# Kernel tuning notes

Hardware: AMD Instinct MI355X
Metric: run time of the kernel (lower is better)

Reference implementation:

```python
import jax, jax.numpy as jnp
import numpy as np

N = 50000
E = 500000
NODE_F = 128
POS_F = 3
COORD_F = 64
EDGE_IN = 2 * NODE_F + 1  # 257


def _linear_params(key, fan_in, fan_out):
    k1, k2 = jax.random.split(key)
    bound = 1.0 / np.sqrt(fan_in)
    W = jax.random.uniform(k1, (fan_in, fan_out), jnp.float32, -bound, bound)
    b = jax.random.uniform(k2, (fan_out,), jnp.float32, -bound, bound)
    return W, b


def setup_inputs() -> dict:
    key = jax.random.key(0)
    ks = jax.random.split(key, 8)
    x = jax.random.normal(ks[0], (N, NODE_F + POS_F), jnp.float32)
    edge_index = jax.random.randint(ks[1], (2, E), 0, N, jnp.int64)
    W_e1, b_e1 = _linear_params(ks[2], EDGE_IN, 2 * EDGE_IN)
    W_e2, b_e2 = _linear_params(ks[3], 2 * EDGE_IN, COORD_F)
    W_c1, b_c1 = _linear_params(ks[4], COORD_F, 4 * COORD_F)
    W_c2, b_c2 = _linear_params(ks[5], 4 * COORD_F, 1)
    W_n1, b_n1 = _linear_params(ks[6], NODE_F + COORD_F, 2 * NODE_F)
    W_n2, b_n2 = _linear_params(ks[7], 2 * NODE_F, NODE_F)
    return {"x": x, "edge_index": edge_index,
            "W_e1": W_e1, "b_e1": b_e1, "W_e2": W_e2, "b_e2": b_e2,
            "W_c1": W_c1, "b_c1": b_c1, "W_c2": W_c2, "b_c2": b_c2,
            "W_n1": W_n1, "b_n1": b_n1, "W_n2": W_n2, "b_n2": b_n2}


def reference(x, edge_index, W_e1, b_e1, W_e2, b_e2, W_c1, b_c1, W_c2, b_c2,
              W_n1, b_n1, W_n2, b_n2):
    node = x[:, :-POS_F]            # (N, 128)
    coords = x[:, -POS_F:]          # (N, 3)
    src = edge_index[0]             # j (source)
    dst = edge_index[1]             # i (target)

    rel_coords = coords[src] - coords[dst]                          # (E, 3)
    rel_dist = jnp.sqrt(jnp.sum(rel_coords ** 2, -1, keepdims=True))  # (E, 1)

    # message: edge_mlp(cat[x_i, x_j, edge_attr])
    e_in = jnp.concatenate([node[dst], node[src], rel_dist], axis=-1)  # (E, 257)
    h = jax.nn.silu(e_in @ W_e1 + b_e1)
    m_ij = jax.nn.silu(h @ W_e2 + b_e2)                             # (E, 64)
    coord_w = jax.nn.silu(m_ij @ W_c1 + b_c1) @ W_c2 + b_c2         # (E, 1)

    # scatter-sum aggregation to target nodes
    m_i = jax.ops.segment_sum(m_ij, dst, num_segments=N)            # (N, 64)
    w_i = jax.ops.segment_sum(coord_w, dst, num_segments=N)         # (N, 1)
    r_i = jax.ops.segment_sum(rel_coords, dst, num_segments=N)      # (N, 3)

    coords_out = coords + w_i * r_i
    n_in = jnp.concatenate([node, m_i], axis=-1)                    # (N, 192)
    hidden = jax.nn.silu(n_in @ W_n1 + b_n1) @ W_n2 + b_n2 + node   # (N, 128)
    return jnp.concatenate([hidden, coords_out], axis=-1)           # (N, 131)
```

## Files before the change

kernel.cpp:

```cpp
#include <hip/hip_runtime.h>
#include <hip/hip_bf16.h>
#include <hip/hip_fp16.h>

#define NN 50000
#define NE 500000
#define DCAP 48

using bf16x8 = __attribute__((ext_vector_type(8))) short;
using f16x8  = __attribute__((ext_vector_type(8))) _Float16;
using f32x4  = __attribute__((ext_vector_type(4))) float;

__device__ __forceinline__ float b2f(unsigned short s) {
  union { unsigned u; float f; } v; v.u = ((unsigned)s) << 16; return v.f;
}
__device__ __forceinline__ unsigned short f2b(float f) {
  __hip_bfloat16 h = __float2bfloat16(f);
  return *reinterpret_cast<unsigned short*>(&h);
}
__device__ __forceinline__ unsigned short f2h(float f) {
  __half h = __float2half(f);
  return *reinterpret_cast<unsigned short*>(&h);
}
__device__ __forceinline__ float hu2f(unsigned short s) {
  __half h; *reinterpret_cast<unsigned short*>(&h) = s; return __half2float(h);
}
__device__ __forceinline__ unsigned pack2(float a, float b) {
  __hip_bfloat162 h = __float22bfloat162_rn(make_float2(a, b));
  return *reinterpret_cast<unsigned*>(&h);
}
__device__ __forceinline__ unsigned pack2h(float a, float b) {
  __half2 h = __float22half2_rn(make_float2(a, b));
  return *reinterpret_cast<unsigned*>(&h);
}
__device__ __forceinline__ __half2 h2u(unsigned u) {
  union { unsigned v; __half2 h; } x; x.v = u; return x.h;
}
__device__ __forceinline__ float silu_f(float x) {
  return x * __fdividef(1.f, 1.f + __expf(-x));
}

__global__ void prep_weights(const float* __restrict__ we1,
                             const float* __restrict__ be1,
                             const float* __restrict__ we2,
                             const float* __restrict__ be2,
                             const float* __restrict__ wc1,
                             const float* __restrict__ wn1,
                             const float* __restrict__ wn2,
                             unsigned short* __restrict__ A1p,
                             unsigned short* __restrict__ A2p,
                             unsigned short* __restrict__ AdB,
                             unsigned short* __restrict__ W2p,
                             unsigned short* __restrict__ Wc1p,
                             unsigned short* __restrict__ Wn1p,
                             unsigned short* __restrict__ Wn2p,
                             float* __restrict__ be1p) {
  int i = blockIdx.x * 256 + threadIdx.x;
  if (i < 67584) {
    int n = i / 128, k = i % 128;
    A1p[i] = (n < 514) ? f2b(we1[k * 514 + n]) : (unsigned short)0;
  } else if (i < 135168) {
    int j = i - 67584; int n = j / 128, k = j % 128;
    A2p[j] = (n < 514) ? f2b(we1[(128 + k) * 514 + n]) : (unsigned short)0;
  } else if (i < 135696) {
    int j = i - 135168;
    AdB[j] = (j < 514) ? f2h(we1[256 * 514 + j]) : (unsigned short)0;
  } else if (i < 170512) {
    int j = i - 135696; int n = j / 544, lk = j % 544;
    unsigned short v = 0;
    if (lk < 514) v = f2h(we2[lk * 64 + n]);
    else if (lk == 514) v = f2h(be2[n]);
    W2p[j] = v;
  } else if (i < 186896) {
    int j = i - 170512; int n = j / 64, k = j % 64;
    Wc1p[j] = f2b(wc1[k * 256 + n]);
  } else if (i < 236048) {
    int j = i - 186896; int n = j / 192, k = j % 192;
    Wn1p[j] = f2b(wn1[k * 256 + n]);
  } else if (i < 268816) {
    int j = i - 236048; int n = j / 256, k = j % 256;
    Wn2p[j] = f2b(wn2[k * 128 + n]);
  } else if (i < 269344) {
    int j = i - 268816;
    be1p[j] = (j < 514) ? be1[j] : 0.f;
  }
}

__global__ void prep_nodes(const float* __restrict__ x,
                           unsigned short* __restrict__ node_p,
                           float* __restrict__ coords_p) {
  int i = blockIdx.x * 256 + threadIdx.x;
  if (i < NN * 16) {
    int g = i >> 4, c = i & 15;
    const float* s = x + g * 131 + c * 8;
    unsigned short* d = node_p + g * 128 + c * 8;
#pragma unroll
    for (int j = 0; j < 8; j++) d[j] = f2b(s[j]);
  } else if (i < NN * 16 + NN) {
    int g = i - NN * 16;
    float4 c;
    c.x = x[g * 131 + 128];
    c.y = x[g * 131 + 129];
    c.z = x[g * 131 + 130];
    c.w = 0.f;
    *(float4*)(coords_p + g * 4) = c;
  }
}

__global__ void build_adj(const int* __restrict__ eidx,
                          int* __restrict__ cnt, int* __restrict__ adj) {
  int e = blockIdx.x * 256 + threadIdx.x;
  if (e < NE) {
    int d = eidx[NE + e];
    d = min(max(d, 0), NN - 1);
    int slot = atomicAdd(&cnt[d], 1);
    if (slot < DCAP) adj[d * DCAP + slot] = e;
  }
}

__launch_bounds__(256, 2)
__global__ void pgemm_kernel(const unsigned short* __restrict__ node_p,
                             const unsigned short* __restrict__ A1p,
                             const unsigned short* __restrict__ A2p,
                             const float* __restrict__ be1p,
                             unsigned short* __restrict__ P1,
                             unsigned short* __restrict__ P2) {
  __shared__ unsigned short sNode[64][136];
  int tid = threadIdx.x, blk = blockIdx.x;
  int lane = tid & 63, wv = tid >> 6, l16 = lane & 15, quad = lane >> 4;
#pragma unroll
  for (int it = 0; it < 4; it++) {
    int t = tid + it * 256;
    int row = t >> 4, ch = t & 15;
    int g = blk * 64 + row;
    if (g >= NN) g = 0;
    *(bf16x8*)(&sNode[row][ch * 8]) = *(const bf16x8*)(node_p + g * 128 + ch * 8);
  }
  __syncthreads();
#pragma unroll 1
  for (int t = 0; t < 9; t++) {
    int T = wv + 4 * t;
    if (T >= 33) break;
    f32x4 a1[4], a2[4];
#pragma unroll
    for (int s = 0; s < 4; s++) {
      a1[s] = (f32x4){0.f, 0.f, 0.f, 0.f};
      a2[s] = (f32x4){0.f, 0.f, 0.f, 0.f};
    }
    for (int kb = 0; kb < 4; kb++) {
      bf16x8 b1 = *(const bf16x8*)(A1p + (T * 16 + l16) * 128 + kb * 32 + quad * 8);
      bf16x8 b2 = *(const bf16x8*)(A2p + (T * 16 + l16) * 128 + kb * 32 + quad * 8);
#pragma unroll
      for (int s = 0; s < 4; s++) {
        bf16x8 a = *(const bf16x8*)(&sNode[s * 16 + l16][kb * 32 + quad * 8]);
        a1[s] = __builtin_amdgcn_mfma_f32_16x16x32_bf16(b1, a, a1[s], 0, 0, 0);
        a2[s] = __builtin_amdgcn_mfma_f32_16x16x32_bf16(b2, a, a2[s], 0, 0, 0);
      }
    }
    int nb = T * 16 + quad * 4;
    float4 b4 = *(const float4*)(be1p + nb);
    bool v0 = nb + 0 < 514, v1 = nb + 1 < 514, v2 = nb + 2 < 514, v3 = nb + 3 < 514;
#pragma unroll
    for (int s = 0; s < 4; s++) {
      int g = blk * 64 + s * 16 + l16;
      if (g < NN) {
        float p0 = v0 ? a1[s][0] + b4.x : 0.f;
        float p1v = v1 ? a1[s][1] + b4.y : 0.f;
        float p2v = v2 ? a1[s][2] + b4.z : 0.f;
        float p3 = v3 ? a1[s][3] + b4.w : 0.f;
        *(uint2*)(P1 + g * 528 + nb) = make_uint2(pack2h(p0, p1v), pack2h(p2v, p3));
        float q0 = v0 ? a2[s][0] : 0.f;
        float q1 = v1 ? a2[s][1] : 0.f;
        float q2 = v2 ? a2[s][2] : 0.f;
        float q3 = v3 ? a2[s][3] : 0.f;
        *(uint2*)(P2 + g * 528 + nb) = make_uint2(pack2h(q0, q1), pack2h(q2, q3));
      }
    }
  }
}

__launch_bounds__(256, 3)
__global__ void edge_kernel(const unsigned short* __restrict__ P1,
                            const unsigned short* __restrict__ P2,
                            const unsigned short* __restrict__ AdB,
                            const float* __restrict__ coords_p,
                            const int* __restrict__ eidx,
                            const unsigned short* __restrict__ W2p,
                            const unsigned short* __restrict__ Wc1p,
                            const float* __restrict__ bc1,
                            const float* __restrict__ bc2,
                            const float* __restrict__ wc2,
                            unsigned short* __restrict__ medge,
                            float* __restrict__ coordw) {
  __shared__ unsigned short sHc[48][168];
  __shared__ unsigned short sM[48][72];
  __shared__ int sDst[48];
  __shared__ int sSrc[48];
  __shared__ float sDistF[48];
  __shared__ float sCwPart[4][48];
  int tid = threadIdx.x, blk = blockIdx.x;
  int lane = tid & 63, wv = tid >> 6, l16 = lane & 15, quad = lane >> 4;

  if (tid < 48) {
    int e = min(blk * 48 + tid, NE - 1);
    int s = eidx[e], d = eidx[NE + e];
    s = min(max(s, 0), NN - 1);
    d = min(max(d, 0), NN - 1);
    float4 cs = *(const float4*)(coords_p + s * 4);
    float4 cd = *(const float4*)(coords_p + d * 4);
    float rx = cs.x - cd.x, ry = cs.y - cd.y, rz = cs.z - cd.z;
    sDst[tid] = d;
    sSrc[tid] = s;
    sDistF[tid] = sqrtf(rx * rx + ry * ry + rz * rz);
  }
  __syncthreads();

  int cg = tid & 15, er = tid >> 4;
  const unsigned short* p1b[3];
  const unsigned short* p2b[3];
  __half2 d2[3];
#pragma unroll
  for (int it = 0; it < 3; it++) {
    int edge = er + it * 16;
    p1b[it] = P1 + sDst[edge] * 528 + cg * 8;
    p2b[it] = P2 + sSrc[edge] * 528 + cg * 8;
    d2[it] = __float2half2_rn(sDistF[edge]);
  }
  const unsigned short* adB = AdB + cg * 8;
  const unsigned short* w2b = W2p + (wv * 16 + l16) * 544 + quad * 8;

  f32x4 macc[3];
#pragma unroll
  for (int s = 0; s < 3; s++) macc[s] = (f32x4){0.f, 0.f, 0.f, 0.f};

#pragma unroll
  for (int ch = 0; ch < 4; ch++) {
    uint4 uva = *(const uint4*)(adB + ch * 128);
    __half2 va0 = h2u(uva.x), va1 = h2u(uva.y), va2 = h2u(uva.z), va3 = h2u(uva.w);
#pragma unroll
    for (int it = 0; it < 3; it++) {
      int edge = er + it * 16;
      uint4 u1 = *(const uint4*)(p1b[it] + ch * 128);
      uint4 u2 = *(const uint4*)(p2b[it] + ch * 128);
      __half2 z0 = __hfma2(va0, d2[it], __hadd2(h2u(u1.x), h2u(u2.x)));
      __half2 z1 = __hfma2(va1, d2[it], __hadd2(h2u(u1.y), h2u(u2.y)));
      __half2 z2 = __hfma2(va2, d2[it], __hadd2(h2u(u1.z), h2u(u2.z)));
      __half2 z3 = __hfma2(va3, d2[it], __hadd2(h2u(u1.w), h2u(u2.w)));
      float f0 = __low2float(z0), f1 = __high2float(z0);
      float f2 = __low2float(z1), f3 = __high2float(z1);
      float f4 = __low2float(z2), f5 = __high2float(z2);
      float f6 = __low2float(z3), f7 = __high2float(z3);
      *(uint4*)(&sHc[edge][cg * 8]) = make_uint4(
          pack2h(silu_f(f0), silu_f(f1)), pack2h(silu_f(f2), silu_f(f3)),
          pack2h(silu_f(f4), silu_f(f5)), pack2h(silu_f(f6), silu_f(f7)));
    }
    if (ch == 3 && tid < 48) {
      int edge = tid;
      float dist = sDistF[edge];
      int bd = sDst[edge] * 528, bs = sSrc[edge] * 528;
      float h512 = silu_f(hu2f(P1[bd + 512]) + hu2f(P2[bs + 512]) + dist * hu2f(AdB[512]));
      float h513 = silu_f(hu2f(P1[bd + 513]) + hu2f(P2[bs + 513]) + dist * hu2f(AdB[513]));
      *(uint4*)(&sHc[edge][128]) = make_uint4(pack2h(h512, h513), pack2h(1.0f, 0.f), 0u, 0u);
      *(uint4*)(&sHc[edge][136]) = make_uint4(0u, 0u, 0u, 0u);
      *(uint4*)(&sHc[edge][144]) = make_uint4(0u, 0u, 0u, 0u);
      *(uint4*)(&sHc[edge][152]) = make_uint4(0u, 0u, 0u, 0u);
    }
    __syncthreads();
    const int nkb = (ch == 3) ? 5 : 4;
#pragma unroll
    for (int kb = 0; kb < nkb; kb++) {
      f16x8 b = *(const f16x8*)(w2b + ch * 128 + kb * 32);
#pragma unroll
      for (int s = 0; s < 3; s++) {
        f16x8 a = *(const f16x8*)(&sHc[s * 16 + l16][kb * 32 + quad * 8]);
        macc[s] = __builtin_amdgcn_mfma_f32_16x16x32_f16(b, a, macc[s], 0, 0, 0);
      }
    }
    __syncthreads();
  }

  {
    int nb = wv * 16 + quad * 4;
#pragma unroll
    for (int s = 0; s < 3; s++) {
      unsigned lo = pack2(silu_f(macc[s][0]), silu_f(macc[s][1]));
      unsigned hi = pack2(silu_f(macc[s][2]), silu_f(macc[s][3]));
      *(uint2*)(&sM[s * 16 + l16][nb]) = make_uint2(lo, hi);
    }
  }
  __syncthreads();

  {
    float cw[3] = {0.f, 0.f, 0.f};
#pragma unroll
    for (int jt = 0; jt < 4; jt++) {
      int T = wv * 4 + jt;
      f32x4 cacc[3];
#pragma unroll
      for (int s = 0; s < 3; s++) cacc[s] = (f32x4){0.f, 0.f, 0.f, 0.f};
#pragma unroll
      for (int kb = 0; kb < 2; kb++) {
        bf16x8 b = *(const bf16x8*)(Wc1p + (T * 16 + l16) * 64 + kb * 32 + quad * 8);
#pragma unroll
        for (int s = 0; s < 3; s++) {
          bf16x8 a = *(const bf16x8*)(&sM[s * 16 + l16][kb * 32 + quad * 8]);
          cacc[s] = __builtin_amdgcn_mfma_f32_16x16x32_bf16(b, a, cacc[s], 0, 0, 0);
        }
      }
      int nb = T * 16 + quad * 4;
      float4 b4 = *(const float4*)(bc1 + nb);
      float4 w4 = *(const float4*)(wc2 + nb);
#pragma unroll
      for (int s = 0; s < 3; s++) {
        cw[s] += silu_f(cacc[s][0] + b4.x) * w4.x;
        cw[s] += silu_f(cacc[s][1] + b4.y) * w4.y;
        cw[s] += silu_f(cacc[s][2] + b4.z) * w4.z;
        cw[s] += silu_f(cacc[s][3] + b4.w) * w4.w;
      }
    }
#pragma unroll
    for (int s = 0; s < 3; s++) {
      cw[s] += __shfl_xor(cw[s], 16, 64);
      cw[s] += __shfl_xor(cw[s], 32, 64);
    }
    if (quad == 0) {
#pragma unroll
      for (int s = 0; s < 3; s++) sCwPart[wv][s * 16 + l16] = cw[s];
    }
  }
  __syncthreads();
#pragma unroll
  for (int it = 0; it < 2; it++) {
    int idx = it * 256 + tid;
    if (idx < 384) {
      int row = idx >> 3, ch8 = idx & 7;
      int e = blk * 48 + row;
      if (e < NE)
        *(bf16x8*)(medge + (size_t)e * 64 + ch8 * 8) = *(const bf16x8*)(&sM[row][ch8 * 8]);
    }
  }
  if (tid < 48) {
    int e = blk * 48 + tid;
    if (e < NE) {
      float v = sCwPart[0][tid] + sCwPart[1][tid] + sCwPart[2][tid] + sCwPart[3][tid]
                + bc2[0];
      coordw[e] = v;
    }
  }
}

__global__ void gather_kernel(const float* __restrict__ coords_p,
                              const unsigned short* __restrict__ medge,
                              const float* __restrict__ coordw,
                              const int* __restrict__ eidx,
                              const int* __restrict__ cnt,
                              const int* __restrict__ adj,
                              float* __restrict__ m_i,
                              float* __restrict__ wr) {
  int t = blockIdx.x * 256 + threadIdx.x;
  int g = t >> 2, c = t & 3;
  if (g >= NN) return;
  int deg = min(cnt[g], DCAP);
  float acc[16];
#pragma unroll
  for (int i = 0; i < 16; i++) acc[i] = 0.f;
  float sc = 0.f;
  float cg = (c < 3) ? coords_p[g * 4 + c] : 0.f;
  for (int k = 0; k < deg; k++) {
    int e = adj[g * DCAP + k];
    const unsigned short* mrow = medge + (size_t)e * 64 + c * 16;
    bf16x8 a0 = *(const bf16x8*)(mrow);
    bf16x8 a1 = *(const bf16x8*)(mrow + 8);
#pragma unroll
    for (int i = 0; i < 8; i++) acc[i] += b2f((unsigned short)a0[i]);
#pragma unroll
    for (int i = 0; i < 8; i++) acc[8 + i] += b2f((unsigned short)a1[i]);
    if (c == 3) {
      sc += coordw[e];
    } else {
      int s = eidx[e];
      s = min(max(s, 0), NN - 1);
      sc += coords_p[s * 4 + c] - cg;
    }
  }
  float4* dst = (float4*)(m_i + g * 64 + c * 16);
  dst[0] = make_float4(acc[0], acc[1], acc[2], acc[3]);
  dst[1] = make_float4(acc[4], acc[5], acc[6], acc[7]);
  dst[2] = make_float4(acc[8], acc[9], acc[10], acc[11]);
  dst[3] = make_float4(acc[12], acc[13], acc[14], acc[15]);
  wr[g * 4 + c] = sc;
}

__launch_bounds__(256, 2)
__global__ void node_mlp_kernel(const unsigned short* __restrict__ node_p,
                                const float* __restrict__ x,
                                const float* __restrict__ coords_p,
                                const float* __restrict__ m_i,
                                const float* __restrict__ wr,
                                const unsigned short* __restrict__ Wn1p,
                                const unsigned short* __restrict__ Wn2p,
                                const float* __restrict__ bn1,
                                const float* __restrict__ bn2,
                                float* __restrict__ out) {
  __shared__ unsigned short sNin[64][200];
  __shared__ unsigned short sHid[64][264];
  int tid = threadIdx.x, blk = blockIdx.x;
  int lane = tid & 63, wv = tid >> 6, l16 = lane & 15, quad = lane >> 4;

#pragma unroll
  for (int it = 0; it < 4; it++) {
    int t = tid + it * 256;
    int row = t >> 4, ch = t & 15;
    int g = blk * 64 + row;
    if (g >= NN) g = 0;
    *(bf16x8*)(&sNin[row][ch * 8]) = *(const bf16x8*)(node_p + g * 128 + ch * 8);
  }
#pragma unroll
  for (int it = 0; it < 2; it++) {
    int t = tid + it * 256;
    int row = t >> 3, q = t & 7;
    int g = blk * 64 + row;
    if (g >= NN) g = 0;
    float4 v1 = *(const float4*)(m_i + g * 64 + q * 8);
    float4 v2 = *(const float4*)(m_i + g * 64 + q * 8 + 4);
    *(uint2*)(&sNin[row][128 + q * 8]) = make_uint2(pack2(v1.x, v1.y), pack2(v1.z, v1.w));
    *(uint2*)(&sNin[row][128 + q * 8 + 4]) = make_uint2(pack2(v2.x, v2.y), pack2(v2.z, v2.w));
  }
  __syncthreads();
  {
    f32x4 acc[4][4];
#pragma unroll
    for (int j = 0; j < 4; j++)
#pragma unroll
      for (int s = 0; s < 4; s++) acc[j][s] = (f32x4){0.f, 0.f, 0.f, 0.f};
    for (int kb = 0; kb < 6; kb++) {
      bf16x8 afr[4], bfr[4];
#pragma unroll
      for (int s = 0; s < 4; s++)
        afr[s] = *(const bf16x8*)(&sNin[s * 16 + l16][kb * 32 + quad * 8]);
#pragma unroll
      for (int j = 0; j < 4; j++)
        bfr[j] = *(const bf16x8*)(Wn1p + ((wv * 4 + j) * 16 + l16) * 192 + kb * 32 + quad * 8);
#pragma unroll
      for (int j = 0; j < 4; j++)
#pragma unroll
        for (int s = 0; s < 4; s++)
          acc[j][s] = __builtin_amdgcn_mfma_f32_16x16x32_bf16(bfr[j], afr[s], acc[j][s], 0, 0, 0);
    }
#pragma unroll
    for (int j = 0; j < 4; j++) {
      int nb = (wv * 4 + j) * 16 + quad * 4;
      float4 b4 = *(const float4*)(bn1 + nb);
#pragma unroll
      for (int s = 0; s < 4; s++) {
        unsigned lo = pack2(silu_f(acc[j][s][0] + b4.x), silu_f(acc[j][s][1] + b4.y));
        unsigned hi = pack2(silu_f(acc[j][s][2] + b4.z), silu_f(acc[j][s][3] + b4.w));
        *(uint2*)(&sHid[s * 16 + l16][nb]) = make_uint2(lo, hi);
      }
    }
  }
  __syncthreads();
  {
    f32x4 acc[2][4];
#pragma unroll
    for (int j = 0; j < 2; j++)
#pragma unroll
      for (int s = 0; s < 4; s++) acc[j][s] = (f32x4){0.f, 0.f, 0.f, 0.f};
    for (int kb = 0; kb < 8; kb++) {
      bf16x8 afr[4], bfr[2];
#pragma unroll
      for (int s = 0; s < 4; s++)
        afr[s] = *(const bf16x8*)(&sHid[s * 16 + l16][kb * 32 + quad * 8]);
#pragma unroll
      for (int j = 0; j < 2; j++)
        bfr[j] = *(const bf16x8*)(Wn2p + ((wv * 2 + j) * 16 + l16) * 256 + kb * 32 + quad * 8);
#pragma unroll
      for (int j = 0; j < 2; j++)
#pragma unroll
        for (int s = 0; s < 4; s++)
          acc[j][s] = __builtin_amdgcn_mfma_f32_16x16x32_bf16(bfr[j], afr[s], acc[j][s], 0, 0, 0);
    }
#pragma unroll
    for (int j = 0; j < 2; j++) {
      int nb = (wv * 2 + j) * 16 + quad * 4;
      float4 b4 = *(const float4*)(bn2 + nb);
#pragma unroll
      for (int s = 0; s < 4; s++) {
        int g = blk * 64 + s * 16 + l16;
        if (g < NN) {
          int base = g * 131 + nb;
          out[base + 0] = acc[j][s][0] + b4.x + x[base + 0];
          out[base + 1] = acc[j][s][1] + b4.y + x[base + 1];
          out[base + 2] = acc[j][s][2] + b4.z + x[base + 2];
          out[base + 3] = acc[j][s][3] + b4.w + x[base + 3];
        }
      }
    }
  }
  if (tid < 64) {
    int g = blk * 64 + tid;
    if (g < NN) {
      float4 w4 = *(const float4*)(wr + g * 4);
      out[g * 131 + 128] = coords_p[g * 4 + 0] + w4.w * w4.x;
      out[g * 131 + 129] = coords_p[g * 4 + 1] + w4.w * w4.y;
      out[g * 131 + 130] = coords_p[g * 4 + 2] + w4.w * w4.z;
    }
  }
}

extern "C" void kernel_launch(void* const* d_in, const int* in_sizes, int n_in,
                              void* d_out, int out_size, void* d_ws, size_t ws_size,
                              hipStream_t stream) {
  const float* x   = (const float*)d_in[0];
  const int* eidx  = (const int*)d_in[1];
  const float* we1 = (const float*)d_in[2];
  const float* be1 = (const float*)d_in[3];
  const float* we2 = (const float*)d_in[4];
  const float* be2 = (const float*)d_in[5];
  const float* wc1 = (const float*)d_in[6];
  const float* bc1 = (const float*)d_in[7];
  const float* wc2 = (const float*)d_in[8];
  const float* bc2 = (const float*)d_in[9];
  const float* wn1 = (const float*)d_in[10];
  const float* bn1 = (const float*)d_in[11];
  const float* wn2 = (const float*)d_in[12];
  const float* bn2 = (const float*)d_in[13];

  char* ws = (char*)d_ws;
  unsigned short* A1p    = (unsigned short*)(ws + 0);
  unsigned short* A2p    = (unsigned short*)(ws + 135168);
  unsigned short* AdB    = (unsigned short*)(ws + 270336);
  unsigned short* W2p    = (unsigned short*)(ws + 271392);
  unsigned short* Wc1p   = (unsigned short*)(ws + 341024);
  unsigned short* Wn1p   = (unsigned short*)(ws + 373792);
  unsigned short* Wn2p   = (unsigned short*)(ws + 472096);
  float* be1p            = (float*)(ws + 537632);
  unsigned short* node_p = (unsigned short*)(ws + 539744);
  float* coords_p        = (float*)(ws + 13339744);
  unsigned short* medge  = (unsigned short*)(ws + 14139744);
  float* coordw          = (float*)(ws + 78139744);
  int* cnt               = (int*)(ws + 80139744);
  int* adj               = (int*)(ws + 80339744);
  float* m_i             = (float*)(ws + 89939744);
  float* wr              = (float*)(ws + 102739744);
  unsigned short* P1     = (unsigned short*)(ws + 103539744);
  unsigned short* P2     = (unsigned short*)(ws + 156339744);

  hipMemsetAsync(cnt, 0, NN * sizeof(int), stream);
  prep_weights<<<(269344 + 255) / 256, 256, 0, stream>>>(we1, be1, we2, be2, wc1,
                                                         wn1, wn2, A1p, A2p, AdB,
                                                         W2p, Wc1p, Wn1p, Wn2p, be1p);
  prep_nodes<<<(NN * 17 + 255) / 256, 256, 0, stream>>>(x, node_p, coords_p);
  pgemm_kernel<<<(NN + 63) / 64, 256, 0, stream>>>(node_p, A1p, A2p, be1p, P1, P2);
  build_adj<<<(NE + 255) / 256, 256, 0, stream>>>(eidx, cnt, adj);
  edge_kernel<<<(NE + 47) / 48, 256, 0, stream>>>(P1, P2, AdB, coords_p, eidx,
                                                  W2p, Wc1p, bc1, bc2, wc2,
                                                  medge, coordw);
  gather_kernel<<<(NN * 4 + 255) / 256, 256, 0, stream>>>(coords_p, medge, coordw,
                                                          eidx, cnt, adj, m_i, wr);
  node_mlp_kernel<<<(NN + 63) / 64, 256, 0, stream>>>(node_p, x, coords_p, m_i, wr,
                                                      Wn1p, Wn2p, bn1, bn2,
                                                      (float*)d_out);
}
```

Before: 508.8 us.

## Sort edges by destination via CSR scan so gather reads contiguous edge rows

Adds a single-block prefix scan over per-node degrees and a compaction kernel that builds a destination-sorted edge order (CSR offsets, edge ids, source ids). The edge kernel now processes edges in that sorted order and writes messages at the sorted position, so the gather kernel reads each node's messages contiguously instead of through random adjacency indirection. This also makes destination-side P1 reads in the edge kernel local. It costs two extra launches, a single-block serial scan, and an extra memset of the order array.

```diff
diff --git a/kernel.cpp b/kernel.cpp
--- a/kernel.cpp
+++ b/kernel.cpp
@@ -117,6 +117,53 @@
   }
 }
 
+__global__ void scan_kernel(const int* __restrict__ cnt, int* __restrict__ off) {
+  __shared__ int part[1024];
+  int tid = threadIdx.x;
+  const int CH = 49;
+  int base = tid * CH;
+  int s = 0;
+  for (int i = 0; i < CH; i++) {
+    int g = base + i;
+    if (g < NN) s += min(cnt[g], DCAP);
+  }
+  part[tid] = s;
+  __syncthreads();
+  for (int d = 1; d < 1024; d <<= 1) {
+    int v = (tid >= d) ? part[tid - d] : 0;
+    __syncthreads();
+    part[tid] += v;
+    __syncthreads();
+  }
+  int run = (tid == 0) ? 0 : part[tid - 1];
+  for (int i = 0; i < CH; i++) {
+    int g = base + i;
+    if (g < NN) {
+      off[g] = run;
+      run += min(cnt[g], DCAP);
+    }
+  }
+  if (tid == 1023) off[NN] = run;
+}
+
+__global__ void compact_adj(const int* __restrict__ cnt,
+                            const int* __restrict__ off,
+                            const int* __restrict__ adj,
+                            const int* __restrict__ eidx,
+                            int* __restrict__ eord,
+                            int* __restrict__ esrc) {
+  int g = blockIdx.x * 256 + threadIdx.x;
+  if (g >= NN) return;
+  int deg = min(cnt[g], DCAP);
+  int o = off[g];
+  for (int k = 0; k < deg; k++) {
+    int e = adj[g * DCAP + k];
+    eord[o + k] = e;
+    int s = eidx[e];
+    esrc[o + k] = min(max(s, 0), NN - 1);
+  }
+}
+
 __launch_bounds__(256, 2)
 __global__ void pgemm_kernel(const unsigned short* __restrict__ node_p,
                              const unsigned short* __restrict__ A1p,
@@ -184,6 +231,7 @@
                             const unsigned short* __restrict__ AdB,
                             const float* __restrict__ coords_p,
                             const int* __restrict__ eidx,
+                            const int* __restrict__ eord,
                             const unsigned short* __restrict__ W2p,
                             const unsigned short* __restrict__ Wc1p,
                             const float* __restrict__ bc1,
@@ -195,13 +243,17 @@
   __shared__ unsigned short sM[48][72];
   __shared__ int sDst[48];
   __shared__ int sSrc[48];
+  __shared__ int sE[48];
   __shared__ float sDistF[48];
   __shared__ float sCwPart[4][48];
   int tid = threadIdx.x, blk = blockIdx.x;
   int lane = tid & 63, wv = tid >> 6, l16 = lane & 15, quad = lane >> 4;
 
   if (tid < 48) {
-    int e = min(blk * 48 + tid, NE - 1);
+    int r = blk * 48 + tid;
+    int e = (r < NE) ? eord[r] : -1;
+    sE[tid] = e;
+    if (e < 0) e = 0;
     int s = eidx[e], d = eidx[NE + e];
     s = min(max(s, 0), NN - 1);
     d = min(max(d, 0), NN - 1);
@@ -333,17 +385,17 @@
     int idx = it * 256 + tid;
     if (idx < 384) {
       int row = idx >> 3, ch8 = idx & 7;
-      int e = blk * 48 + row;
-      if (e < NE)
-        *(bf16x8*)(medge + (size_t)e * 64 + ch8 * 8) = *(const bf16x8*)(&sM[row][ch8 * 8]);
+      int r = blk * 48 + row;
+      if (r < NE && sE[row] >= 0)
+        *(bf16x8*)(medge + (size_t)r * 64 + ch8 * 8) = *(const bf16x8*)(&sM[row][ch8 * 8]);
     }
   }
   if (tid < 48) {
-    int e = blk * 48 + tid;
-    if (e < NE) {
+    int r = blk * 48 + tid;
+    if (r < NE && sE[tid] >= 0) {
       float v = sCwPart[0][tid] + sCwPart[1][tid] + sCwPart[2][tid] + sCwPart[3][tid]
                 + bc2[0];
-      coordw[e] = v;
+      coordw[r] = v;
     }
   }
 }
@@ -351,23 +403,24 @@
 __global__ void gather_kernel(const float* __restrict__ coords_p,
                               const unsigned short* __restrict__ medge,
                               const float* __restrict__ coordw,
-                              const int* __restrict__ eidx,
+                              const int* __restrict__ esrc,
                               const int* __restrict__ cnt,
-                              const int* __restrict__ adj,
+                              const int* __restrict__ off,
                               float* __restrict__ m_i,
                               float* __restrict__ wr) {
   int t = blockIdx.x * 256 + threadIdx.x;
   int g = t >> 2, c = t & 3;
   if (g >= NN) return;
   int deg = min(cnt[g], DCAP);
+  int o = off[g];
   float acc[16];
 #pragma unroll
   for (int i = 0; i < 16; i++) acc[i] = 0.f;
   float sc = 0.f;
   float cg = (c < 3) ? coords_p[g * 4 + c] : 0.f;
   for (int k = 0; k < deg; k++) {
-    int e = adj[g * DCAP + k];
-    const unsigned short* mrow = medge + (size_t)e * 64 + c * 16;
+    int r = o + k;
+    const unsigned short* mrow = medge + (size_t)r * 64 + c * 16;
     bf16x8 a0 = *(const bf16x8*)(mrow);
     bf16x8 a1 = *(const bf16x8*)(mrow + 8);
 #pragma unroll
@@ -375,10 +428,9 @@
 #pragma unroll
     for (int i = 0; i < 8; i++) acc[8 + i] += b2f((unsigned short)a1[i]);
     if (c == 3) {
-      sc += coordw[e];
+      sc += coordw[r];
     } else {
-      int s = eidx[e];
-      s = min(max(s, 0), NN - 1);
+      int s = esrc[r];
       sc += coords_p[s * 4 + c] - cg;
     }
   }
@@ -544,19 +596,25 @@
   float* wr              = (float*)(ws + 102739744);
   unsigned short* P1     = (unsigned short*)(ws + 103539744);
   unsigned short* P2     = (unsigned short*)(ws + 156339744);
+  int* off               = (int*)(ws + 209139744);
+  int* eord              = (int*)(ws + 209339748);
+  int* esrc              = (int*)(ws + 211339748);
 
   hipMemsetAsync(cnt, 0, NN * sizeof(int), stream);
+  hipMemsetAsync(eord, 0xFF, NE * sizeof(int), stream);
   prep_weights<<<(269344 + 255) / 256, 256, 0, stream>>>(we1, be1, we2, be2, wc1,
                                                          wn1, wn2, A1p, A2p, AdB,
                                                          W2p, Wc1p, Wn1p, Wn2p, be1p);
   prep_nodes<<<(NN * 17 + 255) / 256, 256, 0, stream>>>(x, node_p, coords_p);
   pgemm_kernel<<<(NN + 63) / 64, 256, 0, stream>>>(node_p, A1p, A2p, be1p, P1, P2);
   build_adj<<<(NE + 255) / 256, 256, 0, stream>>>(eidx, cnt, adj);
-  edge_kernel<<<(NE + 47) / 48, 256, 0, stream>>>(P1, P2, AdB, coords_p, eidx,
+  scan_kernel<<<1, 1024, 0, stream>>>(cnt, off);
+  compact_adj<<<(NN + 255) / 256, 256, 0, stream>>>(cnt, off, adj, eidx, eord, esrc);
+  edge_kernel<<<(NE + 47) / 48, 256, 0, stream>>>(P1, P2, AdB, coords_p, eidx, eord,
                                                   W2p, Wc1p, bc1, bc2, wc2,
                                                   medge, coordw);
   gather_kernel<<<(NN * 4 + 255) / 256, 256, 0, stream>>>(coords_p, medge, coordw,
-                                                          eidx, cnt, adj, m_i, wr);
+                                                          esrc, cnt, off, m_i, wr);
   node_mlp_kernel<<<(NN + 63) / 64, 256, 0, stream>>>(node_p, x, coords_p, m_i, wr,
                                                       Wn1p, Wn2p, bn1, bn2,
                                                       (float*)d_out);
```

After: 593.0 us. 16.6% more time.
